# Kernel optimization log

Hardware: AMD Instinct MI355X
Metric: run time of the kernel (lower is better)

The kernel has to match this reference:

```python
import jax, jax.numpy as jnp
import numpy as np

D = 128
L_SIZE = 65536
C_SIZE = 32768
E = 262144
N_ITERS = 4


def _mlp(x, w1, b1, w2, b2):
    # 2-layer satbench MLP: Linear -> relu -> Linear
    return jax.nn.relu(x @ w1 + b1) @ w2 + b2


def setup_inputs() -> dict:
    key = jax.random.key(0)
    ks = iter(jax.random.split(key, 32))

    def lin(fi, fo):
        # torch nn.Linear default init, stored as (in, out)
        bound = 1.0 / np.sqrt(fi)
        w = jax.random.uniform(next(ks), (fi, fo), minval=-bound, maxval=bound, dtype=jnp.float32)
        b = jax.random.uniform(next(ks), (fo,), minval=-bound, maxval=bound, dtype=jnp.float32)
        return w, b

    s = np.sqrt(2.0 / D).astype(np.float32)
    inp = {}
    inp['l_edge_index'] = jax.random.randint(next(ks), (E,), 0, L_SIZE, dtype=jnp.int64)
    inp['c_edge_index'] = jax.random.randint(next(ks), (E,), 0, C_SIZE, dtype=jnp.int64)
    inp['l_init'] = jax.random.normal(next(ks), (1, D), dtype=jnp.float32) * s
    inp['c_init'] = jax.random.normal(next(ks), (1, D), dtype=jnp.float32) * s
    inp['w_l2c1'], inp['b_l2c1'] = lin(D, D)
    inp['w_l2c2'], inp['b_l2c2'] = lin(D, D)
    inp['w_c2l1'], inp['b_c2l1'] = lin(D, D)
    inp['w_c2l2'], inp['b_c2l2'] = lin(D, D)
    inp['w_l2l1'], inp['b_l2l1'] = lin(D, D)
    inp['w_l2l2'], inp['b_l2l2'] = lin(D, D)
    inp['w_cu'], inp['b_cu'] = lin(2 * D, D)
    inp['w_lu'], inp['b_lu'] = lin(3 * D, D)
    inp['l_size'] = L_SIZE
    inp['c_size'] = C_SIZE
    return inp


def reference(l_edge_index, c_edge_index, l_init, c_init,
              w_l2c1, b_l2c1, w_l2c2, b_l2c2,
              w_c2l1, b_c2l1, w_c2l2, b_c2l2,
              w_l2l1, b_l2l1, w_l2l2, b_l2l2,
              w_cu, b_cu, w_lu, b_lu, l_size, c_size):
    d = l_init.shape[1]
    ones = jnp.ones((l_edge_index.shape[0], 1), dtype=l_init.dtype)
    l_deg = jax.ops.segment_sum(ones, l_edge_index, num_segments=l_size)   # (L,1)
    c_deg = jax.ops.segment_sum(ones, c_edge_index, num_segments=c_size)   # (C,1)
    degree_norm = jnp.sqrt(l_deg[l_edge_index]) * jnp.sqrt(c_deg[c_edge_index])  # (E,1)

    l_emb = jnp.tile(l_init, (l_size, 1))  # (L,d)
    c_emb = jnp.tile(c_init, (c_size, 1))  # (C,d)

    def step(carry, _):
        l_emb, c_emb = carry
        l2c_msg = _mlp(l_emb, w_l2c1, b_l2c1, w_l2c2, b_l2c2)[l_edge_index]  # (E,d)
        c2l_msg = _mlp(c_emb, w_c2l1, b_c2l1, w_c2l2, b_c2l2)[c_edge_index]  # (E,d)
        # swap positive/negative literal partner embeddings (pairs are adjacent rows)
        l2l_in = l_emb.reshape(l_size // 2, 2, d)[:, ::-1, :].reshape(l_size, d)
        l2l_msg = _mlp(l2l_in, w_l2l1, b_l2l1, w_l2l2, b_l2l2)              # (L,d)
        l2c_aggr = jax.ops.segment_sum(l2c_msg / degree_norm, c_edge_index, num_segments=c_size)
        c_new = jnp.concatenate([c_emb, l2c_aggr], axis=1) @ w_cu + b_cu
        c2l_aggr = jax.ops.segment_sum(c2l_msg / degree_norm, l_edge_index, num_segments=l_size)
        l_new = jnp.concatenate([l_emb, c2l_aggr, l2l_msg], axis=1) @ w_lu + b_lu
        return (l_new, c_new), None

    (l_emb, c_emb), _ = jax.lax.scan(step, (l_emb, c_emb), None, length=N_ITERS)
    return l_emb
```

## Files before the change

### kernel.cpp

```cpp
#include <hip/hip_runtime.h>
#include <hip/hip_bf16.h>

#define D_ 128
#define L_ 65536
#define C_ 32768
#define E_ 262144

typedef __hip_bfloat16 bf16;
typedef __attribute__((ext_vector_type(8))) short short8;
typedef __attribute__((ext_vector_type(4))) float f32x4;

__global__ void detect_k(const unsigned short* __restrict__ wmem,
                         const int* __restrict__ li, int* __restrict__ flags) {
    int t = blockIdx.x * 512 + threadIdx.x;
    if (t < 8192) {
        unsigned short h = wmem[2 * t];
        float v = __bfloat162float(*(const bf16*)&h);
        if (!(fabsf(v) < 0.5f)) atomicOr(&flags[0], 1);
    }
    if (t < 2048) {
        if (li[2 * t + 1] != 0) atomicOr(&flags[1], 1);
    }
}

__device__ __forceinline__ void split2(float v, unsigned short& h, unsigned short& l) {
    bf16 bh = __float2bfloat16(v);
    float fh = __bfloat162float(bh);
    bf16 bl = __float2bfloat16(v - fh);
    h = *(unsigned short*)&bh;
    l = *(unsigned short*)&bl;
}

__device__ __forceinline__ float ldf(const void* s, int i, int isf32) {
    return isf32 ? ((const float*)s)[i] : __bfloat162float(((const bf16*)s)[i]);
}

__global__ void fixdeg_k(const int* __restrict__ ls, const int* __restrict__ cs,
                         int* __restrict__ ld_idx, int* __restrict__ cd_idx,
                         int* __restrict__ ldeg, int* __restrict__ cdeg,
                         const int* __restrict__ flags) {
    int i = blockIdx.x * 256 + threadIdx.x;
    int is32 = flags[1];
    if (i < E_) {
        int v = is32 ? ls[i] : ls[2 * i];
        v = min(max(v, 0), L_ - 1);
        ld_idx[i] = v;
        atomicAdd(&ldeg[v], 1);
    } else {
        int j = i - E_;
        int v = is32 ? cs[j] : cs[2 * j];
        v = min(max(v, 0), C_ - 1);
        cd_idx[j] = v;
        atomicAdd(&cdeg[v], 1);
    }
}

__global__ void cvtwb_k(const void* s0, const void* s1, const void* s2, const void* s3,
                        const void* s4, const void* s5, const void* s6, const void* s7,
                        const void* t0, const void* t1, const void* t2, const void* t3,
                        const void* t4, const void* t5, const void* t6, const void* t7,
                        unsigned short* __restrict__ hi, unsigned short* __restrict__ lo,
                        float* __restrict__ bb, const int* __restrict__ flags) {
    int i = blockIdx.x * 256 + threadIdx.x;
    int isf = flags[0];
    if (i >= 180224) {
        int j = i - 180224;
        const void* src;
        switch (j >> 7) {
            case 0: src = t0; break; case 1: src = t1; break;
            case 2: src = t2; break; case 3: src = t3; break;
            case 4: src = t4; break; case 5: src = t5; break;
            case 6: src = t6; break; default: src = t7; break;
        }
        bb[j] = ldf(src, j & 127, isf);
        return;
    }
    const void* src; int K, base;
    if      (i <  16384) { src = s0; K = 128; base = 0; }
    else if (i <  32768) { src = s1; K = 128; base = 16384; }
    else if (i <  49152) { src = s2; K = 128; base = 32768; }
    else if (i <  65536) { src = s3; K = 128; base = 49152; }
    else if (i <  81920) { src = s4; K = 128; base = 65536; }
    else if (i <  98304) { src = s5; K = 128; base = 81920; }
    else if (i < 131072) { src = s6; K = 256; base = 98304; }
    else                 { src = s7; K = 384; base = 131072; }
    int e = i - base;
    int k = e >> 7, n = e & 127;
    float v = ldf(src, e, isf);
    unsigned short h, l;
    split2(v, h, l);
    hi[base + n * K + k] = h;
    lo[base + n * K + k] = l;
}

__global__ void init2_k(const void* __restrict__ lv, const void* __restrict__ cv,
                        float* __restrict__ lemb, float* __restrict__ cemb,
                        const int* __restrict__ flags) {
    int i4 = blockIdx.x * 256 + threadIdx.x;
    int isf = flags[0];
    const void* src; float* dst; int o;
    if (i4 < L_ * 32) { src = lv; dst = lemb; o = i4; }
    else              { src = cv; dst = cemb; o = i4 - L_ * 32; }
    int j = (o & 31) * 4;
    float4 v;
    v.x = ldf(src, j + 0, isf);
    v.y = ldf(src, j + 1, isf);
    v.z = ldf(src, j + 2, isf);
    v.w = ldf(src, j + 3, isf);
    ((float4*)dst)[o] = v;
}

__global__ void scan1b_k(const int* __restrict__ ldeg, const int* __restrict__ cdeg,
                         int* __restrict__ lout, int* __restrict__ cout,
                         int* __restrict__ bsumL, int* __restrict__ bsumC) {
    __shared__ int s[256];
    const int* in; int* out; int* bs; int tile;
    if (blockIdx.x < 256) { in = ldeg; out = lout; bs = bsumL; tile = blockIdx.x; }
    else                  { in = cdeg; out = cout; bs = bsumC; tile = blockIdx.x - 256; }
    int i = tile * 256 + threadIdx.x;
    int v = in[i];
    s[threadIdx.x] = v;
    __syncthreads();
#pragma unroll
    for (int off = 1; off < 256; off <<= 1) {
        int t = (threadIdx.x >= off) ? s[threadIdx.x - off] : 0;
        __syncthreads();
        s[threadIdx.x] += t;
        __syncthreads();
    }
    out[i] = s[threadIdx.x] - v;
    if (threadIdx.x == 255) bs[tile] = s[255];
}

__global__ void scan2b_k(int* __restrict__ bL, int* __restrict__ bC) {
    __shared__ int s[256];
    int* b = blockIdx.x ? bC : bL;
    int nb = blockIdx.x ? 128 : 256;
    int v = (threadIdx.x < nb) ? b[threadIdx.x] : 0;
    s[threadIdx.x] = v;
    __syncthreads();
#pragma unroll
    for (int off = 1; off < 256; off <<= 1) {
        int t = (threadIdx.x >= off) ? s[threadIdx.x - off] : 0;
        __syncthreads();
        s[threadIdx.x] += t;
        __syncthreads();
    }
    if (threadIdx.x < nb) b[threadIdx.x] = s[threadIdx.x] - v;
}

__global__ void scan3b_k(int* __restrict__ lptr, int* __restrict__ cptr,
                         const int* __restrict__ bsumL, const int* __restrict__ bsumC,
                         int* __restrict__ lcur, int* __restrict__ ccur,
                         const int* __restrict__ ldeg, const int* __restrict__ cdeg,
                         float* __restrict__ invsq_l, float* __restrict__ invsq_c) {
    int b = blockIdx.x, t = threadIdx.x;
    if (b < 256) {
        int i = b * 256 + t;
        int v = lptr[i] + bsumL[b];
        lptr[i] = v; lcur[i] = v;
        int d = ldeg[i];
        invsq_l[i] = d ? rsqrtf((float)d) : 0.0f;
    } else {
        int i = (b - 256) * 256 + t;
        int v = cptr[i] + bsumC[b - 256];
        cptr[i] = v; ccur[i] = v;
        int d = cdeg[i];
        invsq_c[i] = d ? rsqrtf((float)d) : 0.0f;
    }
}

__global__ void place_k(const int* __restrict__ li, const int* __restrict__ ci,
                        int* __restrict__ lcur, int* __restrict__ ccur,
                        int* __restrict__ l_other, int* __restrict__ c_other) {
    int e = blockIdx.x * 256 + threadIdx.x;
    if (e >= E_) return;
    int l = li[e], c = ci[e];
    int p = atomicAdd(&ccur[c], 1);
    c_other[p] = l;
    int q = atomicAdd(&lcur[l], 1);
    l_other[q] = c;
}

__global__ __launch_bounds__(256) void gather2_k(
    const int* __restrict__ cptr, const int* __restrict__ cdeg, const int* __restrict__ c_other,
    const unsigned int* __restrict__ lmsg, const float* __restrict__ invsq_c, float* __restrict__ caggr,
    const int* __restrict__ lptr, const int* __restrict__ ldeg, const int* __restrict__ l_other,
    const unsigned int* __restrict__ cmsg, const float* __restrict__ invsq_l, float* __restrict__ laggr,
    int nC) {
    int node = (blockIdx.x * 256 + threadIdx.x) >> 6;
    int lane = threadIdx.x & 63;
    bool cside = node < nC;
    int j = cside ? node : node - nC;
    const int* ptr = cside ? cptr : lptr;
    const int* dg  = cside ? cdeg : ldeg;
    const int* oth = cside ? c_other : l_other;
    const unsigned int* msg = cside ? lmsg : cmsg;
    float sc = (cside ? invsq_c : invsq_l)[j];
    float* out = cside ? caggr : laggr;
    int s = ptr[j], cnt = dg[j];
    float2 a0 = {0.f, 0.f}, a1 = {0.f, 0.f};
    int k = 0;
    for (; k + 4 <= cnt; k += 4) {
        int o0 = oth[s + k], o1 = oth[s + k + 1], o2 = oth[s + k + 2], o3 = oth[s + k + 3];
        unsigned int u0 = msg[(size_t)o0 * 64 + lane];
        unsigned int u1 = msg[(size_t)o1 * 64 + lane];
        unsigned int u2 = msg[(size_t)o2 * 64 + lane];
        unsigned int u3 = msg[(size_t)o3 * 64 + lane];
        a0.x += __uint_as_float(u0 << 16) + __uint_as_float(u2 << 16);
        a0.y += __uint_as_float(u0 & 0xffff0000u) + __uint_as_float(u2 & 0xffff0000u);
        a1.x += __uint_as_float(u1 << 16) + __uint_as_float(u3 << 16);
        a1.y += __uint_as_float(u1 & 0xffff0000u) + __uint_as_float(u3 & 0xffff0000u);
    }
    for (; k < cnt; k++) {
        int o = oth[s + k];
        unsigned int u = msg[(size_t)o * 64 + lane];
        a0.x += __uint_as_float(u << 16);
        a0.y += __uint_as_float(u & 0xffff0000u);
    }
    a0.x = (a0.x + a1.x) * sc;
    a0.y = (a0.y + a1.y) * sc;
    *(float2*)&out[(size_t)j * D_ + 2 * lane] = a0;
}

__global__ __launch_bounds__(256, 2) void mlp3_k(
    const float* __restrict__ l_cur, const float* __restrict__ c_cur,
    const unsigned short* __restrict__ wt_hi, const unsigned short* __restrict__ wt_lo,
    const float* __restrict__ bb,
    const float* __restrict__ invsq_l, const float* __restrict__ invsq_c,
    bf16* __restrict__ l_msg, bf16* __restrict__ c_msg, bf16* __restrict__ l2lb,
    int nL, int nC) {
    __shared__ char smem[66048];
    unsigned short (*a_hi)[40] = (unsigned short(*)[40])(smem);
    unsigned short (*a_lo)[40] = (unsigned short(*)[40])(smem + 10240);
    unsigned short (*b_hi)[40] = (unsigned short(*)[40])(smem + 20480);
    unsigned short (*b_lo)[40] = (unsigned short(*)[40])(smem + 30720);
    unsigned short* h_hi = (unsigned short*)(smem);
    unsigned short* h_lo = (unsigned short*)(smem + 32768);
    float* scv = (float*)(smem + 65536);

    int b = blockIdx.x, seg, tile;
    if (b < nL)           { seg = 0; tile = b; }
    else if (b < nL + nC) { seg = 1; tile = b - nL; }
    else                  { seg = 2; tile = b - nL - nC; }
    const float* A = (seg == 1) ? c_cur : l_cur;
    bf16* outp = (seg == 0) ? l_msg : (seg == 1) ? c_msg : l2lb;
    const float* invsq = (seg == 0) ? invsq_l : (seg == 1) ? invsq_c : nullptr;
    const unsigned short* W1h = wt_hi + seg * 32768;
    const unsigned short* W1l = wt_lo + seg * 32768;
    const unsigned short* W2h = W1h + 16384;
    const unsigned short* W2l = W1l + 16384;
    const float* b1v = bb + seg * 256;
    const float* b2v = b1v + 128;
    const int swap = (seg == 2);

    const int t = threadIdx.x;
    const int br0 = tile * 128;
    const int w = t >> 6, lane = t & 63;
    const int wr = w >> 1, wc = w & 1;
    const int quad = lane >> 4, cl = lane & 15;

    if (t < 128) scv[t] = invsq ? invsq[br0 + t] : 1.0f;

    f32x4 acc[4][4];
#pragma unroll
    for (int i = 0; i < 4; i++)
#pragma unroll
        for (int j = 0; j < 4; j++) acc[i][j] = (f32x4){0.f, 0.f, 0.f, 0.f};

    for (int kt = 0; kt < 128; kt += 32) {
#pragma unroll
        for (int i = 0; i < 4; i++) {
            int f = t + 256 * i;
            int r = f >> 3, kq = f & 7;
            int gr = br0 + r;
            if (swap) gr ^= 1;
            const float4 v = *(const float4*)&A[(size_t)gr * D_ + kt + 4 * kq];
            unsigned short h0, l0, h1, l1, h2, l2, h3, l3;
            split2(v.x, h0, l0); split2(v.y, h1, l1);
            split2(v.z, h2, l2); split2(v.w, h3, l3);
            *(ushort4*)&a_hi[r][4 * kq] = make_ushort4(h0, h1, h2, h3);
            *(ushort4*)&a_lo[r][4 * kq] = make_ushort4(l0, l1, l2, l3);
            *(ushort4*)&b_hi[r][4 * kq] = *(const ushort4*)&W1h[(size_t)r * 128 + kt + 4 * kq];
            *(ushort4*)&b_lo[r][4 * kq] = *(const ushort4*)&W1l[(size_t)r * 128 + kt + 4 * kq];
        }
        __syncthreads();
        short8 af_h[4], af_l[4];
#pragma unroll
        for (int i = 0; i < 4; i++) {
            int row = 64 * wr + 16 * i + cl;
            af_h[i] = *(const short8*)&a_hi[row][quad * 8];
            af_l[i] = *(const short8*)&a_lo[row][quad * 8];
        }
#pragma unroll
        for (int j = 0; j < 4; j++) {
            int col = 64 * wc + 16 * j + cl;
            short8 bf_h = *(const short8*)&b_hi[col][quad * 8];
            short8 bf_l = *(const short8*)&b_lo[col][quad * 8];
#pragma unroll
            for (int i = 0; i < 4; i++) {
                acc[i][j] = __builtin_amdgcn_mfma_f32_16x16x32_bf16(af_h[i], bf_h, acc[i][j], 0, 0, 0);
                acc[i][j] = __builtin_amdgcn_mfma_f32_16x16x32_bf16(af_h[i], bf_l, acc[i][j], 0, 0, 0);
                acc[i][j] = __builtin_amdgcn_mfma_f32_16x16x32_bf16(af_l[i], bf_h, acc[i][j], 0, 0, 0);
            }
        }
        __syncthreads();
    }
#pragma unroll
    for (int j = 0; j < 4; j++) {
        int col = 64 * wc + 16 * j + cl;
        float bv = b1v[col];
        int g = col >> 3, go = col & 7;
#pragma unroll
        for (int i = 0; i < 4; i++) {
            int rloc = 64 * wr + 16 * i + quad * 4;
#pragma unroll
            for (int rg = 0; rg < 4; rg++) {
                float v = fmaxf(acc[i][j][rg] + bv, 0.0f);
                unsigned short hh, ll;
                split2(v, hh, ll);
                int r = rloc + rg;
                int off = r * 128 + ((g ^ (r & 15)) << 3) + go;
                h_hi[off] = hh;
                h_lo[off] = ll;
            }
        }
    }
    __syncthreads();
#pragma unroll
    for (int i = 0; i < 4; i++)
#pragma unroll
        for (int j = 0; j < 4; j++) acc[i][j] = (f32x4){0.f, 0.f, 0.f, 0.f};

    for (int kt = 0; kt < 128; kt += 32) {
        short8 af_h[4], af_l[4];
        int gbase = (kt >> 3) + quad;
#pragma unroll
        for (int i = 0; i < 4; i++) {
            int r = 64 * wr + 16 * i + cl;
            int off = r * 128 + ((gbase ^ cl) << 3);
            af_h[i] = *(const short8*)&h_hi[off];
            af_l[i] = *(const short8*)&h_lo[off];
        }
#pragma unroll
        for (int j = 0; j < 4; j++) {
            int col = 64 * wc + 16 * j + cl;
            const short8 bf_h = *(const short8*)&W2h[(size_t)col * 128 + kt + quad * 8];
            const short8 bf_l = *(const short8*)&W2l[(size_t)col * 128 + kt + quad * 8];
#pragma unroll
            for (int i = 0; i < 4; i++) {
                acc[i][j] = __builtin_amdgcn_mfma_f32_16x16x32_bf16(af_h[i], bf_h, acc[i][j], 0, 0, 0);
                acc[i][j] = __builtin_amdgcn_mfma_f32_16x16x32_bf16(af_h[i], bf_l, acc[i][j], 0, 0, 0);
                acc[i][j] = __builtin_amdgcn_mfma_f32_16x16x32_bf16(af_l[i], bf_h, acc[i][j], 0, 0, 0);
            }
        }
    }
#pragma unroll
    for (int j = 0; j < 4; j++) {
        int col = 64 * wc + 16 * j + cl;
        float bv = b2v[col];
#pragma unroll
        for (int i = 0; i < 4; i++) {
            int rloc = 64 * wr + 16 * i + quad * 4;
#pragma unroll
            for (int rg = 0; rg < 4; rg++)
                outp[(size_t)(br0 + rloc + rg) * D_ + col] =
                    __float2bfloat16((acc[i][j][rg] + bv) * scv[rloc + rg]);
        }
    }
}

template <int FINAL>
__global__ __launch_bounds__(256, 2) void update_k(
    const float* __restrict__ l_cur, const float* __restrict__ c_cur,
    const float* __restrict__ laggr, const float* __restrict__ caggr,
    const bf16* __restrict__ l2lb,
    const unsigned short* __restrict__ wt_hi, const unsigned short* __restrict__ wt_lo,
    const float* __restrict__ bb,
    float* __restrict__ c_nxt, float* __restrict__ l_nxt,
    void* __restrict__ dout, const int* __restrict__ flags) {
    __shared__ unsigned short a_hi[128][40], a_lo[128][40];
    __shared__ unsigned short b_hi[128][40], b_lo[128][40];
    const int t = threadIdx.x;
    int b = blockIdx.x;
    const bool cseg = (!FINAL) && (b < 256);
    const int tile = (FINAL || cseg) ? b : b - 256;
    const int K = cseg ? 256 : 384;
    const float* A0 = cseg ? c_cur : l_cur;
    const float* A1 = cseg ? caggr : laggr;
    const unsigned short* Wh = wt_hi + (cseg ? 98304 : 131072);
    const unsigned short* Wl = wt_lo + (cseg ? 98304 : 131072);
    const float* bias = bb + (cseg ? 768 : 896);
    const int br0 = tile * 128;
    const int w = t >> 6, lane = t & 63;
    const int wr = w >> 1, wc = w & 1;
    const int quad = lane >> 4, cl = lane & 15;

    f32x4 acc[4][4];
#pragma unroll
    for (int i = 0; i < 4; i++)
#pragma unroll
        for (int j = 0; j < 4; j++) acc[i][j] = (f32x4){0.f, 0.f, 0.f, 0.f};

    for (int kt = 0; kt < K; kt += 32) {
        const bool haslo = (kt < 256);
        const int koff = kt & 127;
#pragma unroll
        for (int i = 0; i < 4; i++) {
            int f = t + 256 * i;
            int r = f >> 3, kq = f & 7;
            if (haslo) {
                const float* As = (kt < 128) ? A0 : A1;
                const float4 v = *(const float4*)&As[(size_t)(br0 + r) * D_ + koff + 4 * kq];
                unsigned short h0, l0, h1, l1, h2, l2, h3, l3;
                split2(v.x, h0, l0); split2(v.y, h1, l1);
                split2(v.z, h2, l2); split2(v.w, h3, l3);
                *(ushort4*)&a_hi[r][4 * kq] = make_ushort4(h0, h1, h2, h3);
                *(ushort4*)&a_lo[r][4 * kq] = make_ushort4(l0, l1, l2, l3);
            } else {
                *(ushort4*)&a_hi[r][4 * kq] =
                    *(const ushort4*)&l2lb[(size_t)(br0 + r) * D_ + koff + 4 * kq];
            }
            *(ushort4*)&b_hi[r][4 * kq] = *(const ushort4*)&Wh[(size_t)r * K + kt + 4 * kq];
            *(ushort4*)&b_lo[r][4 * kq] = *(const ushort4*)&Wl[(size_t)r * K + kt + 4 * kq];
        }
        __syncthreads();
        short8 af_h[4], af_l[4];
#pragma unroll
        for (int i = 0; i < 4; i++) {
            int row = 64 * wr + 16 * i + cl;
            af_h[i] = *(const short8*)&a_hi[row][quad * 8];
            if (haslo) af_l[i] = *(const short8*)&a_lo[row][quad * 8];
        }
#pragma unroll
        for (int j = 0; j < 4; j++) {
            int col = 64 * wc + 16 * j + cl;
            short8 bf_h = *(const short8*)&b_hi[col][quad * 8];
            short8 bf_l = *(const short8*)&b_lo[col][quad * 8];
#pragma unroll
            for (int i = 0; i < 4; i++) {
                acc[i][j] = __builtin_amdgcn_mfma_f32_16x16x32_bf16(af_h[i], bf_h, acc[i][j], 0, 0, 0);
                acc[i][j] = __builtin_amdgcn_mfma_f32_16x16x32_bf16(af_h[i], bf_l, acc[i][j], 0, 0, 0);
                if (haslo)
                    acc[i][j] = __builtin_amdgcn_mfma_f32_16x16x32_bf16(af_l[i], bf_h, acc[i][j], 0, 0, 0);
            }
        }
        __syncthreads();
    }
    const int f32out = FINAL ? flags[0] : 1;
#pragma unroll
    for (int j = 0; j < 4; j++) {
        int col = 64 * wc + 16 * j + cl;
        float bv = bias[col];
#pragma unroll
        for (int i = 0; i < 4; i++) {
            int rbase = br0 + 64 * wr + 16 * i + quad * 4;
#pragma unroll
            for (int rg = 0; rg < 4; rg++) {
                float v = acc[i][j][rg] + bv;
                size_t idx = (size_t)(rbase + rg) * D_ + col;
                if (FINAL) {
                    if (f32out) ((float*)dout)[idx] = v;
                    else        ((bf16*)dout)[idx] = __float2bfloat16(v);
                } else {
                    (cseg ? c_nxt : l_nxt)[idx] = v;
                }
            }
        }
    }
}

extern "C" void kernel_launch(void* const* d_in, const int* in_sizes, int n_in,
                              void* d_out, int out_size, void* d_ws, size_t ws_size,
                              hipStream_t stream) {
    const int* li_raw = (const int*)d_in[0];
    const int* ci_raw = (const int*)d_in[1];

    float* ws = (float*)d_ws;
    float* lbuf0 = ws;
    float* lbuf1 = lbuf0 + (size_t)L_ * D_;
    float* l2lb  = lbuf1 + (size_t)L_ * D_;
    float* laggr = l2lb + (size_t)L_ * D_;
    float* cbuf0 = laggr + (size_t)L_ * D_;
    float* cbuf1 = cbuf0 + (size_t)C_ * D_;
    float* caggr = cbuf1 + (size_t)C_ * D_;
    float* invsq_l = caggr + (size_t)C_ * D_;
    float* invsq_c = invsq_l + L_;
    float* bb    = invsq_c + C_;
    unsigned short* wt_hi = (unsigned short*)(bb + 1024);
    unsigned short* wt_lo = wt_hi + 180224;
    int*   li    = (int*)(wt_lo + 180224);
    int*   ci    = li + E_;
    int*   l_other = ci + E_;
    int*   c_other = l_other + E_;
    int*   ldegi = c_other + E_;
    int*   cdegi = ldegi + L_;
    int*   lptr  = cdegi + C_;
    int*   cptr  = lptr + L_;
    int*   lcur  = cptr + C_;
    int*   ccur  = lcur + L_;
    int*   bsumL = ccur + C_;
    int*   bsumC = bsumL + 256;
    int*   flags = bsumC + 128;

    hipMemsetAsync(flags, 0, 2 * sizeof(int), stream);
    detect_k<<<16, 512, 0, stream>>>((const unsigned short*)d_in[4], li_raw, flags);

    hipMemsetAsync(ldegi, 0, (size_t)(L_ + C_) * sizeof(int), stream);
    fixdeg_k<<<2 * E_ / 256, 256, 0, stream>>>(li_raw, ci_raw, li, ci, ldegi, cdegi, flags);

    cvtwb_k<<<708, 256, 0, stream>>>(d_in[4], d_in[6], d_in[8], d_in[10], d_in[12],
                                     d_in[14], d_in[16], d_in[18],
                                     d_in[5], d_in[7], d_in[9], d_in[11], d_in[13],
                                     d_in[15], d_in[17], d_in[19], wt_hi, wt_lo, bb, flags);

    scan1b_k<<<384, 256, 0, stream>>>(ldegi, cdegi, lptr, cptr, bsumL, bsumC);
    scan2b_k<<<2, 256, 0, stream>>>(bsumL, bsumC);
    scan3b_k<<<384, 256, 0, stream>>>(lptr, cptr, bsumL, bsumC, lcur, ccur,
                                      ldegi, cdegi, invsq_l, invsq_c);
    place_k<<<E_ / 256, 256, 0, stream>>>(li, ci, lcur, ccur, l_other, c_other);

    init2_k<<<(L_ + C_) * 32 / 256, 256, 0, stream>>>(d_in[2], d_in[3], lbuf0, cbuf0, flags);

    float* l_cur = lbuf0; float* l_nxt = lbuf1;
    float* c_cur = cbuf0; float* c_nxt = cbuf1;

    const int nL = L_ / 128, nC = C_ / 128;
    for (int it = 0; it < 3; it++) {
        mlp3_k<<<2 * nL + nC, 256, 0, stream>>>(
            l_cur, c_cur, wt_hi, wt_lo, bb, invsq_l, invsq_c,
            (bf16*)l_nxt, (bf16*)c_nxt, (bf16*)l2lb, nL, nC);
        gather2_k<<<(C_ + L_) / 4, 256, 0, stream>>>(
            cptr, cdegi, c_other, (const unsigned int*)l_nxt, invsq_c, caggr,
            lptr, ldegi, l_other, (const unsigned int*)c_nxt, invsq_l, laggr, C_);
        update_k<0><<<768, 256, 0, stream>>>(
            l_cur, c_cur, laggr, caggr, (const bf16*)l2lb, wt_hi, wt_lo, bb,
            c_nxt, l_nxt, nullptr, flags);
        float* tmp = l_cur; l_cur = l_nxt; l_nxt = tmp;
        tmp = c_cur; c_cur = c_nxt; c_nxt = tmp;
    }
    mlp3_k<<<nC + nL, 256, 0, stream>>>(
        l_cur, c_cur, wt_hi, wt_lo, bb, invsq_l, invsq_c,
        (bf16*)l_nxt, (bf16*)c_nxt, (bf16*)l2lb, 0, nC);
    gather2_k<<<L_ / 4, 256, 0, stream>>>(
        cptr, cdegi, c_other, (const unsigned int*)l_nxt, invsq_c, caggr,
        lptr, ldegi, l_other, (const unsigned int*)c_nxt, invsq_l, laggr, 0);
    update_k<1><<<512, 256, 0, stream>>>(
        l_cur, c_cur, laggr, caggr, (const bf16*)l2lb, wt_hi, wt_lo, bb,
        nullptr, nullptr, d_out, flags);
}
```

Measured before the change: 688.4 us.

## Fold MLP second-layer weights into update weights to shrink update GEMM K

Precomputes the product of each MLP's second-layer weight with the matching slice of the update weight (and the folded biases), so each MLP's output projection is merged into a single pre-multiplied weight. The update kernel now runs only a K=128 GEMM on the current embedding and adds the aggregated and l2l terms elementwise in the epilogue. This removes the K=256/384 concat GEMM work per iteration but relies on the mlp/gather kernels (not shown) now producing pre-projected messages. It also adds a small setup kernel and changes the numerics through re-association.

```diff
diff --git a/kernel.cpp b/kernel.cpp
--- a/kernel.cpp
+++ b/kernel.cpp
@@ -55,42 +55,83 @@
     }
 }
 
-__global__ void cvtwb_k(const void* s0, const void* s1, const void* s2, const void* s3,
-                        const void* s4, const void* s5, const void* s6, const void* s7,
-                        const void* t0, const void* t1, const void* t2, const void* t3,
-                        const void* t4, const void* t5, const void* t6, const void* t7,
-                        unsigned short* __restrict__ hi, unsigned short* __restrict__ lo,
-                        float* __restrict__ bb, const int* __restrict__ flags) {
+__global__ void cvtwb2_k(const void* w1a, const void* w1b, const void* w1c,
+                         const void* wcu, const void* wlu,
+                         const void* w2a, const void* w2b, const void* w2c,
+                         const void* b1a, const void* b2a, const void* b1b, const void* b2b,
+                         const void* b1c, const void* b2c, const void* bcu, const void* blu,
+                         unsigned short* __restrict__ hi, unsigned short* __restrict__ lo,
+                         float* __restrict__ w2f, float* __restrict__ bb,
+                         const int* __restrict__ flags) {
     int i = blockIdx.x * 256 + threadIdx.x;
     int isf = flags[0];
-    if (i >= 180224) {
-        int j = i - 180224;
-        const void* src;
-        switch (j >> 7) {
-            case 0: src = t0; break; case 1: src = t1; break;
-            case 2: src = t2; break; case 3: src = t3; break;
-            case 4: src = t4; break; case 5: src = t5; break;
-            case 6: src = t6; break; default: src = t7; break;
-        }
-        bb[j] = ldf(src, j & 127, isf);
-        return;
-    }
-    const void* src; int K, base;
-    if      (i <  16384) { src = s0; K = 128; base = 0; }
-    else if (i <  32768) { src = s1; K = 128; base = 16384; }
-    else if (i <  49152) { src = s2; K = 128; base = 32768; }
-    else if (i <  65536) { src = s3; K = 128; base = 49152; }
-    else if (i <  81920) { src = s4; K = 128; base = 65536; }
-    else if (i <  98304) { src = s5; K = 128; base = 81920; }
-    else if (i < 131072) { src = s6; K = 256; base = 98304; }
-    else                 { src = s7; K = 384; base = 131072; }
-    int e = i - base;
-    int k = e >> 7, n = e & 127;
-    float v = ldf(src, e, isf);
-    unsigned short h, l;
-    split2(v, h, l);
-    hi[base + n * K + k] = h;
-    lo[base + n * K + k] = l;
+    if (i < 81920) {
+        int jb = i >> 14, e = i & 16383;
+        const void* src; int off;
+        switch (jb) {
+            case 0: src = w1a; off = 0; break;
+            case 1: src = w1b; off = 32768; break;
+            case 2: src = w1c; off = 65536; break;
+            case 3: src = wcu; off = 98304; break;
+            default: src = wlu; off = 114688; break;
+        }
+        float v = ldf(src, e, isf);
+        int k = e >> 7, n = e & 127;
+        unsigned short h, l;
+        split2(v, h, l);
+        hi[off + n * 128 + k] = h;
+        lo[off + n * 128 + k] = l;
+    } else if (i < 180224) {
+        int c = i - 81920;
+        int cb = c >> 14, e = c & 16383;
+        const void* src; int se;
+        switch (cb) {
+            case 0: src = w2a; se = e; break;
+            case 1: src = w2b; se = e; break;
+            case 2: src = w2c; se = e; break;
+            case 3: src = wcu; se = 16384 + e; break;
+            case 4: src = wlu; se = 16384 + e; break;
+            default: src = wlu; se = 32768 + e; break;
+        }
+        w2f[c] = ldf(src, se, isf);
+    } else {
+        int t = i - 180224;
+        int s = t >> 7, o = t & 127;
+        switch (s) {
+            case 0: bb[o]             = ldf(b1a, o, isf); break;
+            case 1: w2f[98304 + o]    = ldf(b2a, o, isf); break;
+            case 2: bb[256 + o]       = ldf(b1b, o, isf); break;
+            case 3: w2f[98432 + o]    = ldf(b2b, o, isf); break;
+            case 4: bb[512 + o]       = ldf(b1c, o, isf); break;
+            case 5: w2f[98560 + o]    = ldf(b2c, o, isf); break;
+            case 6: bb[768 + o]       = ldf(bcu, o, isf); break;
+            default: bb[896 + o]      = ldf(blu, o, isf); break;
+        }
+    }
+}
+
+__global__ void pmul_k(const float* __restrict__ w2f, unsigned short* __restrict__ hi,
+                       unsigned short* __restrict__ lo, float* __restrict__ bb) {
+    int i = blockIdx.x * 256 + threadIdx.x;
+    if (i >= 3 * 129 * 128) return;
+    int seg = i / (129 * 128);
+    int r = i - seg * 129 * 128;
+    int k = r >> 7, n = r & 127;
+    const float* Wu = w2f + 49152 + seg * 16384;
+    float acc = 0.f;
+    if (k < 128) {
+        const float* W2 = w2f + seg * 16384 + k * 128;
+        for (int m = 0; m < 128; m++) acc = fmaf(W2[m], Wu[m * 128 + n], acc);
+        unsigned short h, l;
+        split2(acc, h, l);
+        const int poff = 16384 + seg * 32768;
+        hi[poff + n * 128 + k] = h;
+        lo[poff + n * 128 + k] = l;
+    } else {
+        const float* b2 = w2f + 98304 + seg * 128;
+        for (int m = 0; m < 128; m++) acc = fmaf(b2[m], Wu[m * 128 + n], acc);
+        bb[128 + seg * 256 + n] = acc;
+    }
 }
 
 __global__ void init2_k(const void* __restrict__ lv, const void* __restrict__ cv,
@@ -385,11 +426,10 @@
     int b = blockIdx.x;
     const bool cseg = (!FINAL) && (b < 256);
     const int tile = (FINAL || cseg) ? b : b - 256;
-    const int K = cseg ? 256 : 384;
-    const float* A0 = cseg ? c_cur : l_cur;
-    const float* A1 = cseg ? caggr : laggr;
-    const unsigned short* Wh = wt_hi + (cseg ? 98304 : 131072);
-    const unsigned short* Wl = wt_lo + (cseg ? 98304 : 131072);
+    const float* A = cseg ? c_cur : l_cur;
+    const float* aggr = cseg ? caggr : laggr;
+    const unsigned short* Wh = wt_hi + (cseg ? 98304 : 114688);
+    const unsigned short* Wl = wt_lo + (cseg ? 98304 : 114688);
     const float* bias = bb + (cseg ? 768 : 896);
     const int br0 = tile * 128;
     const int w = t >> 6, lane = t & 63;
@@ -402,27 +442,19 @@
 #pragma unroll
         for (int j = 0; j < 4; j++) acc[i][j] = (f32x4){0.f, 0.f, 0.f, 0.f};
 
-    for (int kt = 0; kt < K; kt += 32) {
-        const bool haslo = (kt < 256);
-        const int koff = kt & 127;
+    for (int kt = 0; kt < 128; kt += 32) {
 #pragma unroll
         for (int i = 0; i < 4; i++) {
             int f = t + 256 * i;
             int r = f >> 3, kq = f & 7;
-            if (haslo) {
-                const float* As = (kt < 128) ? A0 : A1;
-                const float4 v = *(const float4*)&As[(size_t)(br0 + r) * D_ + koff + 4 * kq];
-                unsigned short h0, l0, h1, l1, h2, l2, h3, l3;
-                split2(v.x, h0, l0); split2(v.y, h1, l1);
-                split2(v.z, h2, l2); split2(v.w, h3, l3);
-                *(ushort4*)&a_hi[r][4 * kq] = make_ushort4(h0, h1, h2, h3);
-                *(ushort4*)&a_lo[r][4 * kq] = make_ushort4(l0, l1, l2, l3);
-            } else {
-                *(ushort4*)&a_hi[r][4 * kq] =
-                    *(const ushort4*)&l2lb[(size_t)(br0 + r) * D_ + koff + 4 * kq];
-            }
-            *(ushort4*)&b_hi[r][4 * kq] = *(const ushort4*)&Wh[(size_t)r * K + kt + 4 * kq];
-            *(ushort4*)&b_lo[r][4 * kq] = *(const ushort4*)&Wl[(size_t)r * K + kt + 4 * kq];
+            const float4 v = *(const float4*)&A[(size_t)(br0 + r) * D_ + kt + 4 * kq];
+            unsigned short h0, l0, h1, l1, h2, l2, h3, l3;
+            split2(v.x, h0, l0); split2(v.y, h1, l1);
+            split2(v.z, h2, l2); split2(v.w, h3, l3);
+            *(ushort4*)&a_hi[r][4 * kq] = make_ushort4(h0, h1, h2, h3);
+            *(ushort4*)&a_lo[r][4 * kq] = make_ushort4(l0, l1, l2, l3);
+            *(ushort4*)&b_hi[r][4 * kq] = *(const ushort4*)&Wh[(size_t)r * 128 + kt + 4 * kq];
+            *(ushort4*)&b_lo[r][4 * kq] = *(const ushort4*)&Wl[(size_t)r * 128 + kt + 4 * kq];
         }
         __syncthreads();
         short8 af_h[4], af_l[4];
@@ -430,7 +462,7 @@
         for (int i = 0; i < 4; i++) {
             int row = 64 * wr + 16 * i + cl;
             af_h[i] = *(const short8*)&a_hi[row][quad * 8];
-            if (haslo) af_l[i] = *(const short8*)&a_lo[row][quad * 8];
+            af_l[i] = *(const short8*)&a_lo[row][quad * 8];
         }
 #pragma unroll
         for (int j = 0; j < 4; j++) {
@@ -441,8 +473,7 @@
             for (int i = 0; i < 4; i++) {
                 acc[i][j] = __builtin_amdgcn_mfma_f32_16x16x32_bf16(af_h[i], bf_h, acc[i][j], 0, 0, 0);
                 acc[i][j] = __builtin_amdgcn_mfma_f32_16x16x32_bf16(af_h[i], bf_l, acc[i][j], 0, 0, 0);
-                if (haslo)
-                    acc[i][j] = __builtin_amdgcn_mfma_f32_16x16x32_bf16(af_l[i], bf_h, acc[i][j], 0, 0, 0);
+                acc[i][j] = __builtin_amdgcn_mfma_f32_16x16x32_bf16(af_l[i], bf_h, acc[i][j], 0, 0, 0);
             }
         }
         __syncthreads();
@@ -457,8 +488,9 @@
             int rbase = br0 + 64 * wr + 16 * i + quad * 4;
 #pragma unroll
             for (int rg = 0; rg < 4; rg++) {
-                float v = acc[i][j][rg] + bv;
                 size_t idx = (size_t)(rbase + rg) * D_ + col;
+                float v = acc[i][j][rg] + bv + aggr[idx];
+                if (!cseg) v += __bfloat162float(l2lb[idx]);
                 if (FINAL) {
                     if (f32out) ((float*)dout)[idx] = v;
                     else        ((bf16*)dout)[idx] = __float2bfloat16(v);
@@ -487,9 +519,10 @@
     float* invsq_l = caggr + (size_t)C_ * D_;
     float* invsq_c = invsq_l + L_;
     float* bb    = invsq_c + C_;
-    unsigned short* wt_hi = (unsigned short*)(bb + 1024);
-    unsigned short* wt_lo = wt_hi + 180224;
-    int*   li    = (int*)(wt_lo + 180224);
+    float* w2f   = bb + 1024;
+    unsigned short* wt_hi = (unsigned short*)(w2f + 98688);
+    unsigned short* wt_lo = wt_hi + 131072;
+    int*   li    = (int*)(wt_lo + 131072);
     int*   ci    = li + E_;
     int*   l_other = ci + E_;
     int*   c_other = l_other + E_;
@@ -509,10 +542,12 @@
     hipMemsetAsync(ldegi, 0, (size_t)(L_ + C_) * sizeof(int), stream);
     fixdeg_k<<<2 * E_ / 256, 256, 0, stream>>>(li_raw, ci_raw, li, ci, ldegi, cdegi, flags);
 
-    cvtwb_k<<<708, 256, 0, stream>>>(d_in[4], d_in[6], d_in[8], d_in[10], d_in[12],
-                                     d_in[14], d_in[16], d_in[18],
-                                     d_in[5], d_in[7], d_in[9], d_in[11], d_in[13],
-                                     d_in[15], d_in[17], d_in[19], wt_hi, wt_lo, bb, flags);
+    cvtwb2_k<<<708, 256, 0, stream>>>(d_in[4], d_in[8], d_in[12], d_in[16], d_in[18],
+                                      d_in[6], d_in[10], d_in[14],
+                                      d_in[5], d_in[7], d_in[9], d_in[11],
+                                      d_in[13], d_in[15], d_in[17], d_in[19],
+                                      wt_hi, wt_lo, w2f, bb, flags);
+    pmul_k<<<194, 256, 0, stream>>>(w2f, wt_hi, wt_lo, bb);
 
     scan1b_k<<<384, 256, 0, stream>>>(ldegi, cdegi, lptr, cptr, bsumL, bsumC);
     scan2b_k<<<2, 256, 0, stream>>>(bsumL, bsumC);
```

Result: slower. 710.4 us (+3.2%).

## Restructure MLP kernel into two 64-row halves with direct register operand loads

Applied to the files above, without the earlier changes.

The fused MLP kernel now processes its 128-row tile as two 64-row halves. It loads the A operand and the first-layer weights straight from global memory into MFMA registers instead of staging them through LDS. This shrinks shared memory to 32 KB and halves the accumulator count, so launch bounds rise to 4 blocks per SM, aiming for higher occupancy and fewer LDS round trips and barriers. In exchange, weight fragments are re-read from global/L2 once per half and each wave does redundant uncoalesced loads.

```diff
diff --git a/kernel.cpp b/kernel.cpp
--- a/kernel.cpp
+++ b/kernel.cpp
@@ -29,6 +29,17 @@
     bf16 bl = __float2bfloat16(v - fh);
     h = *(unsigned short*)&bh;
     l = *(unsigned short*)&bl;
+}
+
+__device__ __forceinline__ void split8v(float4 v0, float4 v1, short8& h8, short8& l8) {
+    float vv[8] = {v0.x, v0.y, v0.z, v0.w, v1.x, v1.y, v1.z, v1.w};
+#pragma unroll
+    for (int q = 0; q < 8; q++) {
+        unsigned short h, l;
+        split2(vv[q], h, l);
+        h8[q] = (short)h;
+        l8[q] = (short)l;
+    }
 }
 
 __device__ __forceinline__ float ldf(const void* s, int i, int isf32) {
@@ -223,21 +234,15 @@
     *(float2*)&out[(size_t)j * D_ + 2 * lane] = a0;
 }
 
-__global__ __launch_bounds__(256, 2) void mlp3_k(
+__global__ __launch_bounds__(256, 4) void mlp3_k(
     const float* __restrict__ l_cur, const float* __restrict__ c_cur,
     const unsigned short* __restrict__ wt_hi, const unsigned short* __restrict__ wt_lo,
     const float* __restrict__ bb,
     const float* __restrict__ invsq_l, const float* __restrict__ invsq_c,
     bf16* __restrict__ l_msg, bf16* __restrict__ c_msg, bf16* __restrict__ l2lb,
     int nL, int nC) {
-    __shared__ char smem[66048];
-    unsigned short (*a_hi)[40] = (unsigned short(*)[40])(smem);
-    unsigned short (*a_lo)[40] = (unsigned short(*)[40])(smem + 10240);
-    unsigned short (*b_hi)[40] = (unsigned short(*)[40])(smem + 20480);
-    unsigned short (*b_lo)[40] = (unsigned short(*)[40])(smem + 30720);
-    unsigned short* h_hi = (unsigned short*)(smem);
-    unsigned short* h_lo = (unsigned short*)(smem + 32768);
-    float* scv = (float*)(smem + 65536);
+    __shared__ unsigned short h_hi[64 * 128];
+    __shared__ unsigned short h_lo[64 * 128];
 
     int b = blockIdx.x, seg, tile;
     if (b < nL)           { seg = 0; tile = b; }
@@ -260,112 +265,109 @@
     const int wr = w >> 1, wc = w & 1;
     const int quad = lane >> 4, cl = lane & 15;
 
-    if (t < 128) scv[t] = invsq ? invsq[br0 + t] : 1.0f;
-
-    f32x4 acc[4][4];
-#pragma unroll
-    for (int i = 0; i < 4; i++)
-#pragma unroll
-        for (int j = 0; j < 4; j++) acc[i][j] = (f32x4){0.f, 0.f, 0.f, 0.f};
-
-    for (int kt = 0; kt < 128; kt += 32) {
-#pragma unroll
-        for (int i = 0; i < 4; i++) {
-            int f = t + 256 * i;
-            int r = f >> 3, kq = f & 7;
-            int gr = br0 + r;
-            if (swap) gr ^= 1;
-            const float4 v = *(const float4*)&A[(size_t)gr * D_ + kt + 4 * kq];
-            unsigned short h0, l0, h1, l1, h2, l2, h3, l3;
-            split2(v.x, h0, l0); split2(v.y, h1, l1);
-            split2(v.z, h2, l2); split2(v.w, h3, l3);
-            *(ushort4*)&a_hi[r][4 * kq] = make_ushort4(h0, h1, h2, h3);
-            *(ushort4*)&a_lo[r][4 * kq] = make_ushort4(l0, l1, l2, l3);
-            *(ushort4*)&b_hi[r][4 * kq] = *(const ushort4*)&W1h[(size_t)r * 128 + kt + 4 * kq];
-            *(ushort4*)&b_lo[r][4 * kq] = *(const ushort4*)&W1l[(size_t)r * 128 + kt + 4 * kq];
-        }
-        __syncthreads();
-        short8 af_h[4], af_l[4];
-#pragma unroll
-        for (int i = 0; i < 4; i++) {
-            int row = 64 * wr + 16 * i + cl;
-            af_h[i] = *(const short8*)&a_hi[row][quad * 8];
-            af_l[i] = *(const short8*)&a_lo[row][quad * 8];
-        }
+    for (int half = 0; half < 2; half++) {
+        const int rb = br0 + 64 * half;
+        f32x4 acc[2][4];
+#pragma unroll
+        for (int i = 0; i < 2; i++)
+#pragma unroll
+            for (int j = 0; j < 4; j++) acc[i][j] = (f32x4){0.f, 0.f, 0.f, 0.f};
+
+        for (int kt = 0; kt < 128; kt += 32) {
+            short8 afh[2], afl[2];
+#pragma unroll
+            for (int i = 0; i < 2; i++) {
+                int gr = rb + 32 * wr + 16 * i + cl;
+                if (swap) gr ^= 1;
+                const float* ap = &A[(size_t)gr * D_ + kt + quad * 8];
+                float4 v0 = *(const float4*)ap;
+                float4 v1 = *(const float4*)(ap + 4);
+                split8v(v0, v1, afh[i], afl[i]);
+            }
+#pragma unroll
+            for (int j = 0; j < 4; j++) {
+                int col = 64 * wc + 16 * j + cl;
+                const short8 bfh = *(const short8*)&W1h[(size_t)col * 128 + kt + quad * 8];
+                const short8 bfl = *(const short8*)&W1l[(size_t)col * 128 + kt + quad * 8];
+#pragma unroll
+                for (int i = 0; i < 2; i++) {
+                    acc[i][j] = __builtin_amdgcn_mfma_f32_16x16x32_bf16(afh[i], bfh, acc[i][j], 0, 0, 0);
+                    acc[i][j] = __builtin_amdgcn_mfma_f32_16x16x32_bf16(afh[i], bfl, acc[i][j], 0, 0, 0);
+                    acc[i][j] = __builtin_amdgcn_mfma_f32_16x16x32_bf16(afl[i], bfh, acc[i][j], 0, 0, 0);
+                }
+            }
+        }
+        __syncthreads();
 #pragma unroll
         for (int j = 0; j < 4; j++) {
             int col = 64 * wc + 16 * j + cl;
-            short8 bf_h = *(const short8*)&b_hi[col][quad * 8];
-            short8 bf_l = *(const short8*)&b_lo[col][quad * 8];
-#pragma unroll
-            for (int i = 0; i < 4; i++) {
-                acc[i][j] = __builtin_amdgcn_mfma_f32_16x16x32_bf16(af_h[i], bf_h, acc[i][j], 0, 0, 0);
-                acc[i][j] = __builtin_amdgcn_mfma_f32_16x16x32_bf16(af_h[i], bf_l, acc[i][j], 0, 0, 0);
-                acc[i][j] = __builtin_amdgcn_mfma_f32_16x16x32_bf16(af_l[i], bf_h, acc[i][j], 0, 0, 0);
-            }
-        }
-        __syncthreads();
-    }
-#pragma unroll
-    for (int j = 0; j < 4; j++) {
-        int col = 64 * wc + 16 * j + cl;
-        float bv = b1v[col];
-        int g = col >> 3, go = col & 7;
-#pragma unroll
-        for (int i = 0; i < 4; i++) {
-            int rloc = 64 * wr + 16 * i + quad * 4;
+            float bv = b1v[col];
+            int g = col >> 3, go = col & 7;
+#pragma unroll
+            for (int i = 0; i < 2; i++) {
+                int rloc = 32 * wr + 16 * i + quad * 4;
+#pragma unroll
+                for (int rg = 0; rg < 4; rg++) {
+                    float v = fmaxf(acc[i][j][rg] + bv, 0.0f);
+                    unsigned short hh, ll;
+                    split2(v, hh, ll);
+                    int r = rloc + rg;
+                    int off = r * 128 + ((g ^ (r & 15)) << 3) + go;
+                    h_hi[off] = hh;
+                    h_lo[off] = ll;
+                }
+            }
+        }
+        __syncthreads();
+        f32x4 acc2[2][4];
+#pragma unroll
+        for (int i = 0; i < 2; i++)
+#pragma unroll
+            for (int j = 0; j < 4; j++) acc2[i][j] = (f32x4){0.f, 0.f, 0.f, 0.f};
+
+        for (int kt = 0; kt < 128; kt += 32) {
+            short8 afh[2], afl[2];
+            int gbase = (kt >> 3) + quad;
+#pragma unroll
+            for (int i = 0; i < 2; i++) {
+                int r = 32 * wr + 16 * i + cl;
+                int off = r * 128 + ((gbase ^ cl) << 3);
+                afh[i] = *(const short8*)&h_hi[off];
+                afl[i] = *(const short8*)&h_lo[off];
+            }
+#pragma unroll
+            for (int j = 0; j < 4; j++) {
+                int col = 64 * wc + 16 * j + cl;
+                const short8 bfh = *(const short8*)&W2h[(size_t)col * 128 + kt + quad * 8];
+                const short8 bfl = *(const short8*)&W2l[(size_t)col * 128 + kt + quad * 8];
+#pragma unroll
+                for (int i = 0; i < 2; i++) {
+                    acc2[i][j] = __builtin_amdgcn_mfma_f32_16x16x32_bf16(afh[i], bfh, acc2[i][j], 0, 0, 0);
+                    acc2[i][j] = __builtin_amdgcn_mfma_f32_16x16x32_bf16(afh[i], bfl, acc2[i][j], 0, 0, 0);
+                    acc2[i][j] = __builtin_amdgcn_mfma_f32_16x16x32_bf16(afl[i], bfh, acc2[i][j], 0, 0, 0);
+                }
+            }
+        }
+        float scr[2][4];
+#pragma unroll
+        for (int i = 0; i < 2; i++)
 #pragma unroll
             for (int rg = 0; rg < 4; rg++) {
-                float v = fmaxf(acc[i][j][rg] + bv, 0.0f);
-                unsigned short hh, ll;
-                split2(v, hh, ll);
-                int r = rloc + rg;
-                int off = r * 128 + ((g ^ (r & 15)) << 3) + go;
-                h_hi[off] = hh;
-                h_lo[off] = ll;
-            }
-        }
-    }
-    __syncthreads();
-#pragma unroll
-    for (int i = 0; i < 4; i++)
-#pragma unroll
-        for (int j = 0; j < 4; j++) acc[i][j] = (f32x4){0.f, 0.f, 0.f, 0.f};
-
-    for (int kt = 0; kt < 128; kt += 32) {
-        short8 af_h[4], af_l[4];
-        int gbase = (kt >> 3) + quad;
-#pragma unroll
-        for (int i = 0; i < 4; i++) {
-            int r = 64 * wr + 16 * i + cl;
-            int off = r * 128 + ((gbase ^ cl) << 3);
-            af_h[i] = *(const short8*)&h_hi[off];
-            af_l[i] = *(const short8*)&h_lo[off];
-        }
+                int grow = rb + 32 * wr + 16 * i + quad * 4 + rg;
+                scr[i][rg] = invsq ? invsq[grow] : 1.0f;
+            }
 #pragma unroll
         for (int j = 0; j < 4; j++) {
             int col = 64 * wc + 16 * j + cl;
-            const short8 bf_h = *(const short8*)&W2h[(size_t)col * 128 + kt + quad * 8];
-            const short8 bf_l = *(const short8*)&W2l[(size_t)col * 128 + kt + quad * 8];
-#pragma unroll
-            for (int i = 0; i < 4; i++) {
-                acc[i][j] = __builtin_amdgcn_mfma_f32_16x16x32_bf16(af_h[i], bf_h, acc[i][j], 0, 0, 0);
-                acc[i][j] = __builtin_amdgcn_mfma_f32_16x16x32_bf16(af_h[i], bf_l, acc[i][j], 0, 0, 0);
-                acc[i][j] = __builtin_amdgcn_mfma_f32_16x16x32_bf16(af_l[i], bf_h, acc[i][j], 0, 0, 0);
-            }
-        }
-    }
-#pragma unroll
-    for (int j = 0; j < 4; j++) {
-        int col = 64 * wc + 16 * j + cl;
-        float bv = b2v[col];
-#pragma unroll
-        for (int i = 0; i < 4; i++) {
-            int rloc = 64 * wr + 16 * i + quad * 4;
-#pragma unroll
-            for (int rg = 0; rg < 4; rg++)
-                outp[(size_t)(br0 + rloc + rg) * D_ + col] =
-                    __float2bfloat16((acc[i][j][rg] + bv) * scv[rloc + rg]);
+            float bv = b2v[col];
+#pragma unroll
+            for (int i = 0; i < 2; i++) {
+                int rloc = 32 * wr + 16 * i + quad * 4;
+#pragma unroll
+                for (int rg = 0; rg < 4; rg++)
+                    outp[(size_t)(rb + rloc + rg) * D_ + col] =
+                        __float2bfloat16((acc2[i][j][rg] + bv) * scr[i][rg]);
+            }
         }
     }
 }
```

Result: slower. 1.674 ms (+143.1%).
